# Optimization experiments

Measured on AMD Instinct MI355X. Metric: run time of the kernel, lower is better.

## Reference

```python
import jax, jax.numpy as jnp
import numpy as np

HEADS = 4
DIM_HEAD = 32
DIM = 128
HIDDEN = HEADS * DIM_HEAD  # 128
LN_EPS = 1e-6


def setup_inputs() -> dict:
    key = jax.random.key(0)
    ks = jax.random.split(key, 4)
    b, X, Y, Z = 4, 32, 32, 32
    x = jax.random.normal(ks[0], (b, X, Y, Z, DIM), dtype=jnp.float32)
    # 1x1x1 convs are pointwise linears: kernel [in, out]
    w_qkv = jax.random.normal(ks[1], (DIM, 3 * HIDDEN), dtype=jnp.float32) * (DIM ** -0.5)
    w_out = jax.random.normal(ks[2], (HIDDEN, DIM), dtype=jnp.float32) * (HIDDEN ** -0.5)
    b_out = jax.random.normal(ks[3], (DIM,), dtype=jnp.float32) * 0.02
    ln_scale = jnp.ones((DIM,), dtype=jnp.float32)
    ln_bias = jnp.zeros((DIM,), dtype=jnp.float32)
    return {"x": x, "w_qkv": w_qkv, "w_out": w_out, "b_out": b_out,
            "ln_scale": ln_scale, "ln_bias": ln_bias}


def reference(x, w_qkv, w_out, b_out, ln_scale, ln_bias):
    b, X, Y, Z, c = x.shape
    n = X * Y * Z
    scale = DIM_HEAD ** (-0.5)

    # 1x1x1 conv (no bias) == pointwise matmul over channels
    qkv = jnp.einsum('bxyzc,cd->bxyzd', x, w_qkv)  # [b,X,Y,Z,3*hidden]
    q, k, v = jnp.split(qkv, 3, axis=-1)

    # rearrange 'b x y z (h c) -> b h c n'
    def to_bhcn(t):
        return t.reshape(b, n, HEADS, DIM_HEAD).transpose(0, 2, 3, 1)

    q, k, v = to_bhcn(q), to_bhcn(k), to_bhcn(v)

    q = jax.nn.softmax(q, axis=-2) * scale   # softmax over feature dim d
    k = jax.nn.softmax(k, axis=-1)           # softmax over token dim n

    context = jnp.einsum('bhdn,bhcn->bhdc', k, v)   # [b,h,d,c] small d=c=32
    out = jnp.einsum('bhde,bhdn->bhen', context, q) # [b,h,e,n]

    # rearrange 'b h c n -> b x y z (h c)' (cubic volume, matching original)
    out = out.transpose(0, 3, 1, 2).reshape(b, X, Y, Z, HIDDEN)

    # final 1x1x1 conv with bias
    out = jnp.einsum('bxyzh,hc->bxyzc', out, w_out) + b_out

    # LayerNorm over last axis (flax default eps=1e-6, with scale+bias)
    mu = jnp.mean(out, axis=-1, keepdims=True)
    var = jnp.mean(jnp.square(out - mu), axis=-1, keepdims=True)
    out = (out - mu) * jax.lax.rsqrt(var + LN_EPS) * ln_scale + ln_bias
    return out
```

## Files before the change

### kernel.cpp

```cpp
#include <hip/hip_runtime.h>
#include <hip/hip_bf16.h>

typedef _Float16 f16;
typedef _Float16 f16x4 __attribute__((ext_vector_type(4)));
typedef _Float16 f16x8 __attribute__((ext_vector_type(8)));
typedef float f32x4 __attribute__((ext_vector_type(4)));

#define MFMA(a, b, c) __builtin_amdgcn_mfma_f32_16x16x32_f16((a), (b), (c), 0, 0, 0)

#define BB 4
#define NPOS 32768
#define HH 4
#define NBLK 1024
#define NBLK3 8192
#define STATB 2304
#define LDP 136

__device__ __forceinline__ f16x8 ldx8(const float* p) {
  float4 a = *(const float4*)p;
  float4 b = *(const float4*)(p + 4);
  return (f16x8){(f16)a.x, (f16)a.y, (f16)a.z, (f16)a.w,
                 (f16)b.x, (f16)b.y, (f16)b.z, (f16)b.w};
}

__global__ __launch_bounds__(256)
void la_k0_prep(const float* __restrict__ wqkv, f16* __restrict__ wkvF,
                f16* __restrict__ wqF) {
  const int g0 = blockIdx.x * 256 + threadIdx.x;
  for (int i = g0; i < 32768; i += 16384) {
    int j = i & 7, l = (i >> 3) & 63, ks = (i >> 9) & 3, nt = (i >> 11) & 3,
        h = i >> 13;
    int n = 16 * nt + (l & 15);
    int c = 32 * ks + 8 * (l >> 4) + j;
    int col = (n < 32) ? (128 + h * 32 + n) : (256 + h * 32 + (n - 32));
    wkvF[i] = (f16)wqkv[c * 384 + col];
  }
  {
    int i = g0;
    int j = i & 7, l = (i >> 3) & 63, ks = (i >> 9) & 3, a = (i >> 11) & 1,
        h = i >> 12;
    int row = l & 15;
    int n = 8 * (row >> 2) + 4 * a + (row & 3);
    int c = 32 * ks + 8 * (l >> 4) + j;
    wqF[i] = (f16)wqkv[c * 384 + h * 32 + n];
  }
}

__global__ __launch_bounds__(256, 4)
void la_k1_stats(const float* __restrict__ x, const f16* __restrict__ wkvF,
                 char* __restrict__ stats) {
  const int blk = blockIdx.x, t = threadIdx.x;
  const int w = t >> 6, l = t & 63, lg = l >> 4, ln = l & 15;

  __shared__ __align__(16) f16 EV[2][64 * LDP];

  const float* xb = x + (size_t)blk * (128 * 128);
  f16x8 xf[2][4];
#pragma unroll
  for (int mi = 0; mi < 2; ++mi)
#pragma unroll
    for (int ks = 0; ks < 4; ++ks)
      xf[mi][ks] = ldx8(xb + (32 * w + 16 * mi + ln) * 128 + 32 * ks + 8 * lg);

  const f32x4 Z4 = {0.f, 0.f, 0.f, 0.f};

  auto logits = [&](int h, f32x4 (&acc)[2][4]) {
#pragma unroll
    for (int mi = 0; mi < 2; ++mi)
#pragma unroll
      for (int nt = 0; nt < 4; ++nt) acc[mi][nt] = Z4;
#pragma unroll
    for (int ks = 0; ks < 4; ++ks) {
#pragma unroll
      for (int nt = 0; nt < 4; ++nt) {
        f16x8 bf = *(const f16x8*)(wkvF + (((h * 4 + nt) * 4 + ks) << 9) + l * 8);
        acc[0][nt] = MFMA(xf[0][ks], bf, acc[0][nt]);
        acc[1][nt] = MFMA(xf[1][ks], bf, acc[1][nt]);
      }
    }
  };

  auto phaseA = [&](int h, f32x4 (&acc)[2][4]) {
    f16* E = (f16*)EV[h & 1];
    float sl[2] = {0.f, 0.f};
#pragma unroll
    for (int nt = 0; nt < 2; ++nt)
#pragma unroll
      for (int mi = 0; mi < 2; ++mi) {
        float e0 = __expf(acc[mi][nt][0]);
        float e1 = __expf(acc[mi][nt][1]);
        float e2 = __expf(acc[mi][nt][2]);
        float e3 = __expf(acc[mi][nt][3]);
        sl[nt] += (e0 + e1) + (e2 + e3);
        *(f16x4*)&E[(16 * nt + ln) * LDP + 32 * w + 16 * mi + 4 * lg] =
            (f16x4){(f16)e0, (f16)e1, (f16)e2, (f16)e3};
        f32x4 vv = acc[mi][nt + 2];
        *(f16x4*)&E[(32 + 16 * nt + ln) * LDP + 32 * w + 16 * mi + 4 * lg] =
            (f16x4){(f16)vv[0], (f16)vv[1], (f16)vv[2], (f16)vv[3]};
      }
#pragma unroll
    for (int nt = 0; nt < 2; ++nt) {
      sl[nt] += __shfl_xor(sl[nt], 16);
      sl[nt] += __shfl_xor(sl[nt], 32);
    }
    f16* sp = (f16*)(stats + (size_t)(blk * HH + h) * STATB + 2048);
    if (lg == 0) {
      sp[ln * 4 + w] = (f16)sl[0];
      sp[(16 + ln) * 4 + w] = (f16)sl[1];
    }
  };

  auto phaseB = [&](int h) {
    __syncthreads();
    const f16* E = (const f16*)EV[h & 1];
    const int tm = w >> 1, tn = w & 1;
    f32x4 tacc = Z4;
#pragma unroll
    for (int ks = 0; ks < 4; ++ks) {
      f16x8 ea = *(const f16x8*)&E[(16 * tm + ln) * LDP + 32 * ks + 8 * lg];
      f16x8 vb = *(const f16x8*)&E[(32 + 16 * tn + ln) * LDP + 32 * ks + 8 * lg];
      tacc = MFMA(ea, vb, tacc);
    }
    f16* tp = (f16*)(stats + (size_t)(blk * HH + h) * STATB);
#pragma unroll
    for (int r = 0; r < 4; ++r)
      tp[(16 * tm + 4 * lg + r) * 32 + 16 * tn + ln] = (f16)tacc[r];
  };

  f32x4 accA[2][4], accB[2][4];
  logits(0, accA);
  phaseA(0, accA); logits(1, accB); phaseB(0);
  phaseA(1, accB); logits(2, accA); phaseB(1);
  phaseA(2, accA); logits(3, accB); phaseB(2);
  phaseA(3, accB); phaseB(3);
}

__global__ __launch_bounds__(256)
void la_k2_combine(const char* __restrict__ stats, f16* __restrict__ ctxN) {
  const int gid = blockIdx.x;
  const int bh = gid >> 5, d = gid & 31;
  const int b = bh >> 2, h = bh & 3;
  const int t = threadIdx.x, w = t >> 6, l = t & 63;
  const int c = t & 31, grp = t >> 5;
  __shared__ float redt[4][32];
  __shared__ float reds[4];

  float sg = 0.f, tc = 0.f;
  for (int i = grp; i < 256; i += 8) {
    const char* ub = stats + (size_t)((b * 256 + i) * HH + h) * STATB;
    tc += (float)((const f16*)ub)[d * 32 + c];
    f16x4 s4 = *(const f16x4*)(ub + 2048 + d * 8);
    sg += ((float)s4[0] + (float)s4[1]) + ((float)s4[2] + (float)s4[3]);
  }
  tc += __shfl_xor(tc, 32);
  sg += __shfl_xor(sg, 32);
  if (l < 32) redt[w][l] = tc;
  if (l == 0) reds[w] = sg;
  __syncthreads();
  if (t < 32) {
    float tt = (redt[0][t] + redt[1][t]) + (redt[2][t] + redt[3][t]);
    float ss = (reds[0] + reds[1]) + (reds[2] + reds[3]);
    ctxN[((size_t)bh * 32 + d) * 32 + t] = (f16)(tt / ss);
  }
}

__global__ __launch_bounds__(256)
void la_k2b_fold(const f16* __restrict__ ctxN, const float* __restrict__ wout,
                 f16* __restrict__ GTF) {
  const int b = blockIdx.x, t = threadIdx.x;
  const int h = t >> 6, l = t & 63, lg = l >> 4, ln = l & 15;
  const f32x4 Z4 = {0.f, 0.f, 0.f, 0.f};

  const f16* cb = ctxN + (size_t)((b * HH + h) * 32) * 32;
  f16x8 bfrag[2];
#pragma unroll
  for (int nt = 0; nt < 2; ++nt)
    bfrag[nt] = *(const f16x8*)(cb + (16 * nt + ln) * 32 + 8 * lg);

  f16* gf = GTF + (size_t)b * 16384;
#pragma unroll
  for (int mt = 0; mt < 8; ++mt) {
    f16x8 af;
#pragma unroll
    for (int j = 0; j < 8; ++j)
      af[j] = (f16)wout[(32 * h + 8 * lg + j) * 128 + 16 * mt + ln];
#pragma unroll
    for (int nt = 0; nt < 2; ++nt) {
      f32x4 acc = MFMA(af, bfrag[nt], Z4);
#pragma unroll
      for (int r = 0; r < 4; ++r) {
        int dsub = 16 * nt + ln;
        gf[((h * 8 + mt) << 9) + (16 * (dsub >> 3) + 4 * lg + r) * 8 + (dsub & 7)] =
            (f16)acc[r];
      }
    }
  }
}

__global__ __launch_bounds__(64)
void la_k3_out(const float* __restrict__ x, const f16* __restrict__ wqF,
               const f16* __restrict__ GTF, const float* __restrict__ bout,
               const float* __restrict__ lns, const float* __restrict__ lnb,
               float* __restrict__ out) {
  const int blk = blockIdx.x;
  const int l = threadIdx.x, lg = l >> 4, ln = l & 15;
  const int b = blk >> 11;
  const int p0 = blk * 16;

  const float* xb = x + (size_t)p0 * 128;
  f16x8 xf[4];
#pragma unroll
  for (int ks = 0; ks < 4; ++ks)
    xf[ks] = ldx8(xb + ln * 128 + 32 * ks + 8 * lg);

  const f32x4 Z4 = {0.f, 0.f, 0.f, 0.f};
  const f16* gf = GTF + (size_t)b * 16384;

  f32x4 y[8];
#pragma unroll
  for (int nc = 0; nc < 8; ++nc) y[nc] = Z4;

  auto qlog = [&](int h, f32x4 (&qa)[2]) {
    qa[0] = Z4;
    qa[1] = Z4;
#pragma unroll
    for (int ks = 0; ks < 4; ++ks) {
      f16x8 a0 = *(const f16x8*)(wqF + (((h * 2 + 0) * 4 + ks) << 9) + l * 8);
      f16x8 a1 = *(const f16x8*)(wqF + (((h * 2 + 1) * 4 + ks) << 9) + l * 8);
      qa[0] = MFMA(a0, xf[ks], qa[0]);
      qa[1] = MFMA(a1, xf[ks], qa[1]);
    }
  };

  auto consume = [&](f32x4 (&qa)[2], f16x8& af) {
    float s = 0.f;
#pragma unroll
    for (int mt = 0; mt < 2; ++mt)
#pragma unroll
      for (int r = 0; r < 4; ++r) {
        qa[mt][r] = __expf(qa[mt][r]);
        s += qa[mt][r];
      }
    s += __shfl_xor(s, 16);
    s += __shfl_xor(s, 32);
    const float inv = 0.17677669529663688f / s;
    af = (f16x8){(f16)(qa[0][0] * inv), (f16)(qa[0][1] * inv),
                 (f16)(qa[0][2] * inv), (f16)(qa[0][3] * inv),
                 (f16)(qa[1][0] * inv), (f16)(qa[1][1] * inv),
                 (f16)(qa[1][2] * inv), (f16)(qa[1][3] * inv)};
  };

  auto ymfma = [&](int h, f16x8& af) {
#pragma unroll
    for (int nc = 0; nc < 8; ++nc) {
      f16x8 gfr = *(const f16x8*)(gf + (((h * 8 + nc) << 9) + l * 8));
      y[nc] = MFMA(gfr, af, y[nc]);
    }
  };

  f32x4 qaA[2], qaB[2];
  f16x8 afA, afB;
  qlog(0, qaA); qlog(1, qaB);
  consume(qaA, afA); ymfma(0, afA); qlog(2, qaA);
  consume(qaB, afB); ymfma(1, afB); qlog(3, qaB);
  consume(qaA, afA); ymfma(2, afA);
  consume(qaB, afB); ymfma(3, afB);

#pragma unroll
  for (int nc = 0; nc < 8; ++nc) {
    f32x4 bb = *(const f32x4*)(bout + 16 * nc + 4 * lg);
    y[nc] += bb;
  }

  float s = 0.f;
#pragma unroll
  for (int nc = 0; nc < 8; ++nc)
    s += (y[nc][0] + y[nc][1]) + (y[nc][2] + y[nc][3]);
  s += __shfl_xor(s, 16);
  s += __shfl_xor(s, 32);
  const float mean = s * (1.f / 128.f);
  float v = 0.f;
#pragma unroll
  for (int nc = 0; nc < 8; ++nc)
#pragma unroll
    for (int r = 0; r < 4; ++r) {
      float dv = y[nc][r] - mean;
      v = fmaf(dv, dv, v);
    }
  v += __shfl_xor(v, 16);
  v += __shfl_xor(v, 32);
  const float inv = rsqrtf(v * (1.f / 128.f) + 1e-6f);

  float* op = out + (size_t)(p0 + ln) * 128;
#pragma unroll
  for (int nc = 0; nc < 8; ++nc) {
    f32x4 sv = *(const f32x4*)(lns + 16 * nc + 4 * lg);
    f32x4 b2 = *(const f32x4*)(lnb + 16 * nc + 4 * lg);
    f32x4 o4;
#pragma unroll
    for (int r = 0; r < 4; ++r)
      o4[r] = (y[nc][r] - mean) * inv * sv[r] + b2[r];
    *(f32x4*)(op + 16 * nc + 4 * lg) = o4;
  }
}

extern "C" void kernel_launch(void* const* d_in, const int* in_sizes, int n_in,
                              void* d_out, int out_size, void* d_ws, size_t ws_size,
                              hipStream_t stream) {
  const float* x = (const float*)d_in[0];
  const float* w_qkv = (const float*)d_in[1];
  const float* w_out = (const float*)d_in[2];
  const float* b_out = (const float*)d_in[3];
  const float* ln_s = (const float*)d_in[4];
  const float* ln_b = (const float*)d_in[5];
  float* out = (float*)d_out;

  char* ws = (char*)d_ws;
  char* stats = ws;
  f16* wkvF = (f16*)(ws + 9437184);
  f16* wqF = (f16*)(ws + 9437184 + 65536);
  f16* GTF = (f16*)(ws + 9437184 + 65536 + 32768);
  f16* ctxN = (f16*)(ws + 9437184 + 65536 + 32768 + 131072);

  la_k0_prep<<<dim3(64), 256, 0, stream>>>(w_qkv, wkvF, wqF);
  la_k1_stats<<<dim3(NBLK), 256, 0, stream>>>(x, wkvF, stats);
  la_k2_combine<<<dim3(512), 256, 0, stream>>>(stats, ctxN);
  la_k2b_fold<<<dim3(BB), 256, 0, stream>>>(ctxN, w_out, GTF);
  la_k3_out<<<dim3(NBLK3), 64, 0, stream>>>(x, wqF, GTF, b_out, ln_s, ln_b, out);
}
```

Baseline: 87.43 us.

## Compute softmaxed Q in stats kernel and stream fp16 Q to output kernel

The Q projection and its feature-dim softmax move into the first pass, which already has x loaded in registers. The result is written as fp16 MFMA fragments to a new workspace buffer. The output kernel no longer rereads the fp32 x (64 MB) and instead reads the fp16 Q (32 MB). It also processes two 16-row groups per block, so it launches half as many blocks. This trades an extra 32 MB write in the first pass for less read traffic and less exp work in the last pass, and adds register pressure to the stats kernel.

```diff
diff --git a/kernel.cpp b/kernel.cpp
--- a/kernel.cpp
+++ b/kernel.cpp
@@ -12,7 +12,7 @@
 #define NPOS 32768
 #define HH 4
 #define NBLK 1024
-#define NBLK3 8192
+#define NBLK3 4096
 #define STATB 2304
 #define LDP 136
 
@@ -48,7 +48,8 @@
 
 __global__ __launch_bounds__(256, 4)
 void la_k1_stats(const float* __restrict__ x, const f16* __restrict__ wkvF,
-                 char* __restrict__ stats) {
+                 const f16* __restrict__ wqF, char* __restrict__ stats,
+                 f16* __restrict__ Qhat) {
   const int blk = blockIdx.x, t = threadIdx.x;
   const int w = t >> 6, l = t & 63, lg = l >> 4, ln = l & 15;
 
@@ -77,6 +78,46 @@
         acc[0][nt] = MFMA(xf[0][ks], bf, acc[0][nt]);
         acc[1][nt] = MFMA(xf[1][ks], bf, acc[1][nt]);
       }
+    }
+  };
+
+  auto qlog = [&](int h, f32x4 (&qa)[2][2]) {
+#pragma unroll
+    for (int mi = 0; mi < 2; ++mi)
+#pragma unroll
+      for (int a = 0; a < 2; ++a) qa[mi][a] = Z4;
+#pragma unroll
+    for (int ks = 0; ks < 4; ++ks) {
+      f16x8 a0 = *(const f16x8*)(wqF + (((h * 2 + 0) * 4 + ks) << 9) + l * 8);
+      f16x8 a1 = *(const f16x8*)(wqF + (((h * 2 + 1) * 4 + ks) << 9) + l * 8);
+#pragma unroll
+      for (int mi = 0; mi < 2; ++mi) {
+        qa[mi][0] = MFMA(a0, xf[mi][ks], qa[mi][0]);
+        qa[mi][1] = MFMA(a1, xf[mi][ks], qa[mi][1]);
+      }
+    }
+  };
+
+  auto qfin = [&](int h, f32x4 (&qa)[2][2]) {
+#pragma unroll
+    for (int mi = 0; mi < 2; ++mi) {
+      float s = 0.f;
+#pragma unroll
+      for (int a = 0; a < 2; ++a)
+#pragma unroll
+        for (int r = 0; r < 4; ++r) {
+          qa[mi][a][r] = __expf(qa[mi][a][r]);
+          s += qa[mi][a][r];
+        }
+      s += __shfl_xor(s, 16);
+      s += __shfl_xor(s, 32);
+      const float inv = 0.17677669529663688f / s;
+      f16x8 af = (f16x8){(f16)(qa[mi][0][0] * inv), (f16)(qa[mi][0][1] * inv),
+                         (f16)(qa[mi][0][2] * inv), (f16)(qa[mi][0][3] * inv),
+                         (f16)(qa[mi][1][0] * inv), (f16)(qa[mi][1][1] * inv),
+                         (f16)(qa[mi][1][2] * inv), (f16)(qa[mi][1][3] * inv)};
+      f16* qp = Qhat + (((size_t)(blk * 8 + 2 * w + mi) * 4 + h) << 9) + l * 8;
+      *(f16x8*)qp = af;
     }
   };
 
@@ -127,12 +168,12 @@
       tp[(16 * tm + 4 * lg + r) * 32 + 16 * tn + ln] = (f16)tacc[r];
   };
 
-  f32x4 accA[2][4], accB[2][4];
+  f32x4 accA[2][4], accB[2][4], qa[2][2];
   logits(0, accA);
-  phaseA(0, accA); logits(1, accB); phaseB(0);
-  phaseA(1, accB); logits(2, accA); phaseB(1);
-  phaseA(2, accA); logits(3, accB); phaseB(2);
-  phaseA(3, accB); phaseB(3);
+  phaseA(0, accA); qlog(0, qa); qfin(0, qa); logits(1, accB); phaseB(0);
+  phaseA(1, accB); qlog(1, qa); qfin(1, qa); logits(2, accA); phaseB(1);
+  phaseA(2, accA); qlog(2, qa); qfin(2, qa); logits(3, accB); phaseB(2);
+  phaseA(3, accB); qlog(3, qa); qfin(3, qa); phaseB(3);
 }
 
 __global__ __launch_bounds__(256)
@@ -198,109 +239,79 @@
 }
 
 __global__ __launch_bounds__(64)
-void la_k3_out(const float* __restrict__ x, const f16* __restrict__ wqF,
-               const f16* __restrict__ GTF, const float* __restrict__ bout,
-               const float* __restrict__ lns, const float* __restrict__ lnb,
-               float* __restrict__ out) {
+void la_k3_out(const f16* __restrict__ Qhat, const f16* __restrict__ GTF,
+               const float* __restrict__ bout, const float* __restrict__ lns,
+               const float* __restrict__ lnb, float* __restrict__ out) {
   const int blk = blockIdx.x;
   const int l = threadIdx.x, lg = l >> 4, ln = l & 15;
-  const int b = blk >> 11;
-  const int p0 = blk * 16;
-
-  const float* xb = x + (size_t)p0 * 128;
-  f16x8 xf[4];
-#pragma unroll
-  for (int ks = 0; ks < 4; ++ks)
-    xf[ks] = ldx8(xb + ln * 128 + 32 * ks + 8 * lg);
+  const int b = blk >> 10;
 
   const f32x4 Z4 = {0.f, 0.f, 0.f, 0.f};
   const f16* gf = GTF + (size_t)b * 16384;
 
-  f32x4 y[8];
-#pragma unroll
-  for (int nc = 0; nc < 8; ++nc) y[nc] = Z4;
-
-  auto qlog = [&](int h, f32x4 (&qa)[2]) {
-    qa[0] = Z4;
-    qa[1] = Z4;
-#pragma unroll
-    for (int ks = 0; ks < 4; ++ks) {
-      f16x8 a0 = *(const f16x8*)(wqF + (((h * 2 + 0) * 4 + ks) << 9) + l * 8);
-      f16x8 a1 = *(const f16x8*)(wqF + (((h * 2 + 1) * 4 + ks) << 9) + l * 8);
-      qa[0] = MFMA(a0, xf[ks], qa[0]);
-      qa[1] = MFMA(a1, xf[ks], qa[1]);
-    }
-  };
-
-  auto consume = [&](f32x4 (&qa)[2], f16x8& af) {
+  f16x8 af[2][4];
+#pragma unroll
+  for (int g = 0; g < 2; ++g)
+#pragma unroll
+    for (int h = 0; h < HH; ++h)
+      af[g][h] = *(const f16x8*)(Qhat +
+          (((size_t)(blk * 2 + g) * 4 + h) << 9) + l * 8);
+
+  f32x4 y[2][8];
+#pragma unroll
+  for (int g = 0; g < 2; ++g)
+#pragma unroll
+    for (int nc = 0; nc < 8; ++nc) y[g][nc] = Z4;
+
+#pragma unroll
+  for (int h = 0; h < HH; ++h) {
+#pragma unroll
+    for (int nc = 0; nc < 8; ++nc) {
+      f16x8 gfr = *(const f16x8*)(gf + (((h * 8 + nc) << 9) + l * 8));
+      y[0][nc] = MFMA(gfr, af[0][h], y[0][nc]);
+      y[1][nc] = MFMA(gfr, af[1][h], y[1][nc]);
+    }
+  }
+
+#pragma unroll
+  for (int nc = 0; nc < 8; ++nc) {
+    f32x4 bb = *(const f32x4*)(bout + 16 * nc + 4 * lg);
+    y[0][nc] += bb;
+    y[1][nc] += bb;
+  }
+
+#pragma unroll
+  for (int g = 0; g < 2; ++g) {
     float s = 0.f;
 #pragma unroll
-    for (int mt = 0; mt < 2; ++mt)
-#pragma unroll
-      for (int r = 0; r < 4; ++r) {
-        qa[mt][r] = __expf(qa[mt][r]);
-        s += qa[mt][r];
-      }
+    for (int nc = 0; nc < 8; ++nc)
+      s += (y[g][nc][0] + y[g][nc][1]) + (y[g][nc][2] + y[g][nc][3]);
     s += __shfl_xor(s, 16);
     s += __shfl_xor(s, 32);
-    const float inv = 0.17677669529663688f / s;
-    af = (f16x8){(f16)(qa[0][0] * inv), (f16)(qa[0][1] * inv),
-                 (f16)(qa[0][2] * inv), (f16)(qa[0][3] * inv),
-                 (f16)(qa[1][0] * inv), (f16)(qa[1][1] * inv),
-                 (f16)(qa[1][2] * inv), (f16)(qa[1][3] * inv)};
-  };
-
-  auto ymfma = [&](int h, f16x8& af) {
+    const float mean = s * (1.f / 128.f);
+    float v = 0.f;
+#pragma unroll
+    for (int nc = 0; nc < 8; ++nc)
+#pragma unroll
+      for (int r = 0; r < 4; ++r) {
+        float dv = y[g][nc][r] - mean;
+        v = fmaf(dv, dv, v);
+      }
+    v += __shfl_xor(v, 16);
+    v += __shfl_xor(v, 32);
+    const float inv = rsqrtf(v * (1.f / 128.f) + 1e-6f);
+
+    float* op = out + (size_t)(blk * 32 + 16 * g + ln) * 128;
 #pragma unroll
     for (int nc = 0; nc < 8; ++nc) {
-      f16x8 gfr = *(const f16x8*)(gf + (((h * 8 + nc) << 9) + l * 8));
-      y[nc] = MFMA(gfr, af, y[nc]);
-    }
-  };
-
-  f32x4 qaA[2], qaB[2];
-  f16x8 afA, afB;
-  qlog(0, qaA); qlog(1, qaB);
-  consume(qaA, afA); ymfma(0, afA); qlog(2, qaA);
-  consume(qaB, afB); ymfma(1, afB); qlog(3, qaB);
-  consume(qaA, afA); ymfma(2, afA);
-  consume(qaB, afB); ymfma(3, afB);
-
-#pragma unroll
-  for (int nc = 0; nc < 8; ++nc) {
-    f32x4 bb = *(const f32x4*)(bout + 16 * nc + 4 * lg);
-    y[nc] += bb;
-  }
-
-  float s = 0.f;
-#pragma unroll
-  for (int nc = 0; nc < 8; ++nc)
-    s += (y[nc][0] + y[nc][1]) + (y[nc][2] + y[nc][3]);
-  s += __shfl_xor(s, 16);
-  s += __shfl_xor(s, 32);
-  const float mean = s * (1.f / 128.f);
-  float v = 0.f;
-#pragma unroll
-  for (int nc = 0; nc < 8; ++nc)
-#pragma unroll
-    for (int r = 0; r < 4; ++r) {
-      float dv = y[nc][r] - mean;
-      v = fmaf(dv, dv, v);
-    }
-  v += __shfl_xor(v, 16);
-  v += __shfl_xor(v, 32);
-  const float inv = rsqrtf(v * (1.f / 128.f) + 1e-6f);
-
-  float* op = out + (size_t)(p0 + ln) * 128;
-#pragma unroll
-  for (int nc = 0; nc < 8; ++nc) {
-    f32x4 sv = *(const f32x4*)(lns + 16 * nc + 4 * lg);
-    f32x4 b2 = *(const f32x4*)(lnb + 16 * nc + 4 * lg);
-    f32x4 o4;
-#pragma unroll
-    for (int r = 0; r < 4; ++r)
-      o4[r] = (y[nc][r] - mean) * inv * sv[r] + b2[r];
-    *(f32x4*)(op + 16 * nc + 4 * lg) = o4;
+      f32x4 sv = *(const f32x4*)(lns + 16 * nc + 4 * lg);
+      f32x4 b2 = *(const f32x4*)(lnb + 16 * nc + 4 * lg);
+      f32x4 o4;
+#pragma unroll
+      for (int r = 0; r < 4; ++r)
+        o4[r] = (y[g][nc][r] - mean) * inv * sv[r] + b2[r];
+      *(f32x4*)(op + 16 * nc + 4 * lg) = o4;
+    }
   }
 }
 
@@ -321,10 +332,11 @@
   f16* wqF = (f16*)(ws + 9437184 + 65536);
   f16* GTF = (f16*)(ws + 9437184 + 65536 + 32768);
   f16* ctxN = (f16*)(ws + 9437184 + 65536 + 32768 + 131072);
+  f16* Qhat = (f16*)(ws + 9437184 + 65536 + 32768 + 131072 + 32768);
 
   la_k0_prep<<<dim3(64), 256, 0, stream>>>(w_qkv, wkvF, wqF);
-  la_k1_stats<<<dim3(NBLK), 256, 0, stream>>>(x, wkvF, stats);
+  la_k1_stats<<<dim3(NBLK), 256, 0, stream>>>(x, wkvF, wqF, stats, Qhat);
   la_k2_combine<<<dim3(512), 256, 0, stream>>>(stats, ctxN);
   la_k2b_fold<<<dim3(BB), 256, 0, stream>>>(ctxN, w_out, GTF);
-  la_k3_out<<<dim3(NBLK3), 64, 0, stream>>>(x, wqF, GTF, b_out, ln_s, ln_b, out);
-}
+  la_k3_out<<<dim3(NBLK3), 64, 0, stream>>>(Qhat, GTF, b_out, ln_s, ln_b, out);
+}
```

After: 77.58 us. 11.3% less time.
